# Performance work log

Measured on AMD Instinct MI355X. Metric: run time of the kernel, lower is better.

The kernel has to match this reference:

```python
import jax, jax.numpy as jnp
import numpy as np

N_NODES = 50000
N_EDGES = 1600000
IN_DIM = 1024
MID_DIM = 256


def setup_inputs() -> dict:
    key = jax.random.key(0)
    k1, k2, k3, k4 = jax.random.split(key, 4)
    x = jax.random.normal(k1, (N_NODES, IN_DIM), dtype=jnp.float32)
    edge_index = jax.random.randint(k2, (2, N_EDGES), 0, N_NODES, dtype=jnp.int64)
    # Glorot-style init like PyG GCNConv
    W1 = jax.random.normal(k3, (IN_DIM, MID_DIM), dtype=jnp.float32) * (2.0 / (IN_DIM + MID_DIM)) ** 0.5
    W2 = jax.random.normal(k4, (MID_DIM, IN_DIM), dtype=jnp.float32) * (2.0 / (MID_DIM + IN_DIM)) ** 0.5
    b1 = jnp.zeros((MID_DIM,), dtype=jnp.float32)
    b2 = jnp.zeros((IN_DIM,), dtype=jnp.float32)
    return {"x": x, "edge_index": edge_index, "W1": W1, "b1": b1, "W2": W2, "b2": b2}


def _gcn_conv(x, W, b, src, dst, norm, n):
    # PyG GCNConv: linear transform first, then normalized neighbor sum, then bias.
    xw = x @ W                                   # [N, F_out]
    msg = xw[src] * norm[:, None]                # gather + scale, [E+N, F_out]
    out = jax.ops.segment_sum(msg, dst, num_segments=n)
    return out + b


def reference(x, edge_index, W1, b1, W2, b2):
    n = x.shape[0]
    loops = jnp.arange(n, dtype=edge_index.dtype)
    src = jnp.concatenate([edge_index[0], loops])
    dst = jnp.concatenate([edge_index[1], loops])
    # symmetric normalization with self-loops: D^-1/2 (A+I) D^-1/2
    deg = jax.ops.segment_sum(jnp.ones_like(dst, dtype=x.dtype), dst, num_segments=n)
    dis = jnp.where(deg > 0, jax.lax.rsqrt(jnp.maximum(deg, 1.0)), 0.0)
    norm = dis[src] * dis[dst]                   # [E+N]
    h = jax.nn.relu(_gcn_conv(x, W1, b1, src, dst, norm, n))
    # F.dropout(training=False) is identity at inference
    out = _gcn_conv(h, W2, b2, src, dst, norm, n)
    return out
```

## Files before the change

kernel.cpp:

```cpp
#include <hip/hip_runtime.h>

typedef unsigned short u16;
typedef u16 u16x8 __attribute__((ext_vector_type(8)));
typedef u16 u16x4 __attribute__((ext_vector_type(4)));
typedef short s16x8 __attribute__((ext_vector_type(8)));
typedef float f32x4 __attribute__((ext_vector_type(4)));

__device__ __forceinline__ float b2f(u16 u) {
  unsigned int v = ((unsigned int)u) << 16;
  return __builtin_bit_cast(float, v);
}
__device__ __forceinline__ u16 f2b(float f) {
  unsigned int u = __builtin_bit_cast(unsigned int, f);
  u += 0x7FFFu + ((u >> 16) & 1u);
  return (u16)(u >> 16);
}

__device__ __forceinline__ void gld16(void* lds, const void* g) {
  __builtin_amdgcn_global_load_lds(
      (const __attribute__((address_space(1))) void*)g,
      (__attribute__((address_space(3))) void*)lds, 16, 0, 0);
}

__global__ void deg_kernel(const int* __restrict__ dst, int* __restrict__ deg, int E, int n) {
  int e = blockIdx.x * 256 + threadIdx.x;
  if (e < E) {
    int d = dst[e];
    d = min(max(d, 0), n - 1);
    atomicAdd(&deg[d], 1);
  }
}

__global__ void dis_kernel(const int* __restrict__ deg, float* __restrict__ dis, int n) {
  int i = blockIdx.x * 256 + threadIdx.x;
  if (i < n) dis[i] = 1.0f / sqrtf((float)(deg[i] + 1));
}

__global__ __launch_bounds__(256) void scanA(const int* __restrict__ cnt, int* __restrict__ bsum, int n) {
  __shared__ int s[256];
  int t = threadIdx.x, i = blockIdx.x * 256 + t;
  s[t] = (i < n) ? cnt[i] : 0;
  __syncthreads();
  for (int off = 128; off > 0; off >>= 1) {
    if (t < off) s[t] += s[t + off];
    __syncthreads();
  }
  if (t == 0) bsum[blockIdx.x] = s[0];
}

__global__ __launch_bounds__(256) void scanB(int* __restrict__ bsum, int nb) {
  __shared__ int s[256];
  int t = threadIdx.x;
  int v = (t < nb) ? bsum[t] : 0;
  s[t] = v;
  __syncthreads();
  for (int off = 1; off < 256; off <<= 1) {
    int x = (t >= off) ? s[t - off] : 0;
    __syncthreads();
    s[t] += x;
    __syncthreads();
  }
  if (t < nb) bsum[t] = s[t] - v;
}

__global__ __launch_bounds__(256) void scanC(const int* __restrict__ cnt, const int* __restrict__ bsum,
                                             int* __restrict__ rowp, int n) {
  __shared__ int s[256];
  int t = threadIdx.x, i = blockIdx.x * 256 + t;
  int v = (i < n) ? cnt[i] : 0;
  s[t] = v;
  __syncthreads();
  for (int off = 1; off < 256; off <<= 1) {
    int x = (t >= off) ? s[t - off] : 0;
    __syncthreads();
    s[t] += x;
    __syncthreads();
  }
  if (i < n) rowp[i + 1] = bsum[blockIdx.x] + s[t];
  if (i == 0) rowp[0] = 0;
}

__global__ void fill_kernel(const int* __restrict__ src, const int* __restrict__ dst,
                            const int* __restrict__ rowp, int* __restrict__ fill,
                            const float* __restrict__ dis, int* __restrict__ csr_s,
                            float* __restrict__ csr_w, int E, int n) {
  int e = blockIdx.x * 256 + threadIdx.x;
  if (e < E) {
    int s = src[e]; s = min(max(s, 0), n - 1);
    int d = dst[e]; d = min(max(d, 0), n - 1);
    int pos = rowp[d] + atomicAdd(&fill[d], 1);
    csr_s[pos] = s;
    csr_w[pos] = dis[s] * dis[d];
  }
}

__global__ void transpose_cvt(const float* __restrict__ in, u16* __restrict__ out, int K, int N) {
  int idx = blockIdx.x * 256 + threadIdx.x;
  if (idx < K * N) {
    int k = idx / N, nn = idx - k * N;
    out[(size_t)nn * K + k] = f2b(in[idx]);
  }
}

template <bool A_F32, bool OUT_F32>
__global__ __launch_bounds__(256) void gemm_m97(const void* __restrict__ Ap,
                                                const u16* __restrict__ BT,
                                                const float* __restrict__ bias,
                                                void* __restrict__ Cp, int M, int N, int K) {
  constexpr int ABYTES = A_F32 ? 16384 : 8192;
  __shared__ alignas(16) unsigned char smem[ABYTES + 8192];
  unsigned char* Asm = smem;
  unsigned char* Bsm = smem + ABYTES;

  const int tid = threadIdx.x;
  const int m0 = blockIdx.y * 128, n0 = blockIdx.x * 128;
  const int lane = tid & 63, wv = tid >> 6;
  const int wr = (wv >> 1) * 64, wc = (wv & 1) * 64;
  const int q = lane >> 4, l = lane & 15;
  f32x4 acc[4][4] = {};

  constexpr int NA = A_F32 ? 4 : 2;
  constexpr size_t AB = A_F32 ? 4 : 2;
  const char* a_src[NA];
  const char* b_src[2];
#pragma unroll
  for (int i = 0; i < NA; i++) {
    int c = tid + i * 256;
    int r, lb;
    if (A_F32) {
      r = c >> 3;
      int sb = (c & 7) * 16;
      lb = sb ^ ((r & 7) << 4);
    } else {
      r = c >> 2;
      int sb = (c & 3) * 16;
      lb = sb ^ ((r & 3) << 4);
    }
    int gr = m0 + r;
    if (gr > M - 1) gr = M - 1;
    a_src[i] = (const char*)Ap + (size_t)gr * K * AB + lb;
  }
#pragma unroll
  for (int i = 0; i < 2; i++) {
    int c = tid + i * 256;
    int r = c >> 2;
    int sb = (c & 3) * 16;
    int lb = sb ^ ((r & 3) << 4);
    b_src[i] = (const char*)BT + (size_t)(n0 + r) * K * 2 + lb;
  }

  for (int kt = 0; kt < K; kt += 32) {
#pragma unroll
    for (int i = 0; i < NA; i++)
      gld16(Asm + (tid + i * 256) * 16, a_src[i] + (size_t)kt * AB);
#pragma unroll
    for (int i = 0; i < 2; i++)
      gld16(Bsm + (tid + i * 256) * 16, b_src[i] + (size_t)kt * 2);
    __syncthreads();

    s16x8 af[4], bf[4];
    if (A_F32) {
#pragma unroll
      for (int mi = 0; mi < 4; mi++) {
        int R = wr + mi * 16 + l;
        int xr = (R & 7) << 4;
        const char* rb = (const char*)Asm + R * 128;
        float4 lo = *(const float4*)(rb + ((q * 32) ^ xr));
        float4 hi = *(const float4*)(rb + ((q * 32 + 16) ^ xr));
        unsigned int d0, d1, d2, d3;
        asm("v_cvt_pk_bf16_f32 %0, %1, %2" : "=v"(d0) : "v"(lo.x), "v"(lo.y));
        asm("v_cvt_pk_bf16_f32 %0, %1, %2" : "=v"(d1) : "v"(lo.z), "v"(lo.w));
        asm("v_cvt_pk_bf16_f32 %0, %1, %2" : "=v"(d2) : "v"(hi.x), "v"(hi.y));
        asm("v_cvt_pk_bf16_f32 %0, %1, %2" : "=v"(d3) : "v"(hi.z), "v"(hi.w));
        int4 di;
        di.x = (int)d0; di.y = (int)d1; di.z = (int)d2; di.w = (int)d3;
        af[mi] = __builtin_bit_cast(s16x8, di);
      }
    } else {
#pragma unroll
      for (int mi = 0; mi < 4; mi++) {
        int R = wr + mi * 16 + l;
        af[mi] = *(const s16x8*)((const char*)Asm + R * 64 + ((q * 16) ^ ((R & 3) << 4)));
      }
    }
#pragma unroll
    for (int ni = 0; ni < 4; ni++) {
      int C = wc + ni * 16 + l;
      bf[ni] = *(const s16x8*)((const char*)Bsm + C * 64 + ((q * 16) ^ ((C & 3) << 4)));
    }

#pragma unroll
    for (int mi = 0; mi < 4; mi++)
#pragma unroll
      for (int ni = 0; ni < 4; ni++)
        acc[mi][ni] = __builtin_amdgcn_mfma_f32_16x16x32_bf16(af[mi], bf[ni], acc[mi][ni], 0, 0, 0);
    __syncthreads();
  }

#pragma unroll
  for (int ni = 0; ni < 4; ni++) {
    int col = n0 + wc + ni * 16 + l;
    float bv = bias ? bias[col] : 0.f;
#pragma unroll
    for (int mi = 0; mi < 4; mi++) {
#pragma unroll
      for (int j = 0; j < 4; j++) {
        int row = m0 + wr + mi * 16 + q * 4 + j;
        if (row < M) {
          float v = acc[mi][ni][j] + bv;
          if (OUT_F32)
            ((float*)Cp)[(size_t)row * N + col] = v;
          else
            ((u16*)Cp)[(size_t)row * N + col] = f2b(v);
        }
      }
    }
  }
}

template <bool RELU>
__global__ __launch_bounds__(256) void agg_kernel(const u16* __restrict__ tab,
                                                  const int* __restrict__ rowp,
                                                  const int* __restrict__ csr_s,
                                                  const float* __restrict__ csr_w,
                                                  const float* __restrict__ dis,
                                                  const float* __restrict__ bias,
                                                  u16* __restrict__ out, int n) {
  int wv = threadIdx.x >> 6, lane = threadIdx.x & 63;
  int node = blockIdx.x * 4 + wv;
  if (node >= n) return;
  int f0 = lane * 4;
  float sw = dis[node];
  sw *= sw;
  u16x4 v = *(const u16x4*)&tab[(size_t)node * 256 + f0];
  float a0 = sw * b2f(v[0]), a1 = sw * b2f(v[1]), a2 = sw * b2f(v[2]), a3 = sw * b2f(v[3]);
  int e0 = rowp[node], e1 = rowp[node + 1];
  int e = e0;
  for (; e + 4 <= e1; e += 4) {
    int s0 = csr_s[e], s1 = csr_s[e + 1], s2 = csr_s[e + 2], s3 = csr_s[e + 3];
    float w0 = csr_w[e], w1 = csr_w[e + 1], w2 = csr_w[e + 2], w3 = csr_w[e + 3];
    u16x4 u0 = *(const u16x4*)&tab[(size_t)s0 * 256 + f0];
    u16x4 u1 = *(const u16x4*)&tab[(size_t)s1 * 256 + f0];
    u16x4 u2 = *(const u16x4*)&tab[(size_t)s2 * 256 + f0];
    u16x4 u3 = *(const u16x4*)&tab[(size_t)s3 * 256 + f0];
    a0 += w0 * b2f(u0[0]) + w1 * b2f(u1[0]) + w2 * b2f(u2[0]) + w3 * b2f(u3[0]);
    a1 += w0 * b2f(u0[1]) + w1 * b2f(u1[1]) + w2 * b2f(u2[1]) + w3 * b2f(u3[1]);
    a2 += w0 * b2f(u0[2]) + w1 * b2f(u1[2]) + w2 * b2f(u2[2]) + w3 * b2f(u3[2]);
    a3 += w0 * b2f(u0[3]) + w1 * b2f(u1[3]) + w2 * b2f(u2[3]) + w3 * b2f(u3[3]);
  }
  for (; e < e1; e++) {
    int s = csr_s[e];
    float w = csr_w[e];
    u16x4 u = *(const u16x4*)&tab[(size_t)s * 256 + f0];
    a0 += w * b2f(u[0]);
    a1 += w * b2f(u[1]);
    a2 += w * b2f(u[2]);
    a3 += w * b2f(u[3]);
  }
  if (RELU) {
    a0 = fmaxf(a0 + bias[f0 + 0], 0.f);
    a1 = fmaxf(a1 + bias[f0 + 1], 0.f);
    a2 = fmaxf(a2 + bias[f0 + 2], 0.f);
    a3 = fmaxf(a3 + bias[f0 + 3], 0.f);
  }
  u16x4 o;
  o[0] = f2b(a0); o[1] = f2b(a1); o[2] = f2b(a2); o[3] = f2b(a3);
  *(u16x4*)&out[(size_t)node * 256 + f0] = o;
}

extern "C" void kernel_launch(void* const* d_in, const int* in_sizes, int n_in,
                              void* d_out, int out_size, void* d_ws, size_t ws_size,
                              hipStream_t stream) {
  const float* x  = (const float*)d_in[0];
  const int*   ei = (const int*)d_in[1];
  const float* W1 = (const float*)d_in[2];
  const float* b1 = (const float*)d_in[3];
  const float* W2 = (const float*)d_in[4];
  const float* b2 = (const float*)d_in[5];

  const int MID = in_sizes[3];
  const int IN  = in_sizes[5];
  const int n   = in_sizes[0] / IN;
  const int E   = in_sizes[1] / 2;
  const int* srcv = ei;
  const int* dstv = ei + E;

  char* w = (char*)d_ws;
  size_t off = 0;
  auto alloc = [&](size_t bytes) -> void* {
    void* p = w + off;
    off += (bytes + 255) & ~(size_t)255;
    return p;
  };
  int*   deg   = (int*)alloc((size_t)n * 4);
  int*   rowp  = (int*)alloc((size_t)(n + 1) * 4);
  int*   fill  = (int*)alloc((size_t)n * 4);
  int*   bsum  = (int*)alloc(1024);
  int*   csr_s = (int*)alloc((size_t)E * 4);
  float* csr_w = (float*)alloc((size_t)E * 4);
  float* dis   = (float*)alloc((size_t)n * 4);
  u16*   W1T   = (u16*)alloc((size_t)IN * MID * 2);
  u16*   W2T   = (u16*)alloc((size_t)IN * MID * 2);
  u16*   xw    = (u16*)alloc((size_t)n * MID * 2);
  u16*   h     = (u16*)alloc((size_t)n * MID * 2);
  u16*   ah    = xw;

  hipMemsetAsync(deg, 0, (size_t)n * 4, stream);
  hipMemsetAsync(fill, 0, (size_t)n * 4, stream);

  transpose_cvt<<<(IN * MID + 255) / 256, 256, 0, stream>>>(W1, W1T, IN, MID);
  transpose_cvt<<<(IN * MID + 255) / 256, 256, 0, stream>>>(W2, W2T, MID, IN);

  const int nb = (n + 255) / 256;
  deg_kernel<<<(E + 255) / 256, 256, 0, stream>>>(dstv, deg, E, n);
  dis_kernel<<<nb, 256, 0, stream>>>(deg, dis, n);
  scanA<<<nb, 256, 0, stream>>>(deg, bsum, n);
  scanB<<<1, 256, 0, stream>>>(bsum, nb);
  scanC<<<nb, 256, 0, stream>>>(deg, bsum, rowp, n);
  fill_kernel<<<(E + 255) / 256, 256, 0, stream>>>(srcv, dstv, rowp, fill, dis, csr_s, csr_w, E, n);

  dim3 g1(MID / 128, (n + 127) / 128);
  gemm_m97<true, false><<<g1, 256, 0, stream>>>(x, W1T, nullptr, xw, n, MID, IN);
  agg_kernel<true><<<(n + 3) / 4, 256, 0, stream>>>(xw, rowp, csr_s, csr_w, dis, b1, h, n);
  agg_kernel<false><<<(n + 3) / 4, 256, 0, stream>>>(h, rowp, csr_s, csr_w, dis, nullptr, ah, n);
  dim3 g2(IN / 128, (n + 127) / 128);
  gemm_m97<false, true><<<g2, 256, 0, stream>>>(ah, W2T, b2, d_out, n, IN, MID);
}
```

Baseline: 891.2 us.

## Replace 4-wave 128x128 GEMM with single-wave 64x64 tiles without block barriers

Both dense GEMMs move from 256-thread blocks computing 128x128 tiles to one-wave blocks computing 64x64 tiles. Because a block is now a single wave, the __syncthreads barriers are replaced by an explicit vmcnt wait plus a scheduling barrier. The aim is to cut barrier stalls and raise the number of independently scheduled blocks. In exchange, each tile reuses loaded data less, so the large fp32 input and the weights are fetched more times. There is also still no double buffering, so loads and MFMA work stay serialized within each wave.

```diff
diff --git a/kernel.cpp b/kernel.cpp
--- a/kernel.cpp
+++ b/kernel.cpp
@@ -103,29 +103,27 @@
 }
 
 template <bool A_F32, bool OUT_F32>
-__global__ __launch_bounds__(256) void gemm_m97(const void* __restrict__ Ap,
-                                                const u16* __restrict__ BT,
-                                                const float* __restrict__ bias,
-                                                void* __restrict__ Cp, int M, int N, int K) {
-  constexpr int ABYTES = A_F32 ? 16384 : 8192;
-  __shared__ alignas(16) unsigned char smem[ABYTES + 8192];
+__global__ __launch_bounds__(64) void gemm_w64(const void* __restrict__ Ap,
+                                               const u16* __restrict__ BT,
+                                               const float* __restrict__ bias,
+                                               void* __restrict__ Cp, int M, int N, int K) {
+  constexpr int ABYTES = A_F32 ? 8192 : 4096;
+  __shared__ alignas(16) unsigned char smem[ABYTES + 4096];
   unsigned char* Asm = smem;
   unsigned char* Bsm = smem + ABYTES;
 
-  const int tid = threadIdx.x;
-  const int m0 = blockIdx.y * 128, n0 = blockIdx.x * 128;
-  const int lane = tid & 63, wv = tid >> 6;
-  const int wr = (wv >> 1) * 64, wc = (wv & 1) * 64;
+  const int lane = threadIdx.x;
+  const int m0 = blockIdx.y * 64, n0 = blockIdx.x * 64;
   const int q = lane >> 4, l = lane & 15;
   f32x4 acc[4][4] = {};
 
-  constexpr int NA = A_F32 ? 4 : 2;
+  constexpr int NA = A_F32 ? 8 : 4;
   constexpr size_t AB = A_F32 ? 4 : 2;
   const char* a_src[NA];
-  const char* b_src[2];
+  const char* b_src[4];
 #pragma unroll
   for (int i = 0; i < NA; i++) {
-    int c = tid + i * 256;
+    int c = lane + i * 64;
     int r, lb;
     if (A_F32) {
       r = c >> 3;
@@ -141,8 +139,8 @@
     a_src[i] = (const char*)Ap + (size_t)gr * K * AB + lb;
   }
 #pragma unroll
-  for (int i = 0; i < 2; i++) {
-    int c = tid + i * 256;
+  for (int i = 0; i < 4; i++) {
+    int c = lane + i * 64;
     int r = c >> 2;
     int sb = (c & 3) * 16;
     int lb = sb ^ ((r & 3) << 4);
@@ -152,17 +150,18 @@
   for (int kt = 0; kt < K; kt += 32) {
 #pragma unroll
     for (int i = 0; i < NA; i++)
-      gld16(Asm + (tid + i * 256) * 16, a_src[i] + (size_t)kt * AB);
-#pragma unroll
-    for (int i = 0; i < 2; i++)
-      gld16(Bsm + (tid + i * 256) * 16, b_src[i] + (size_t)kt * 2);
-    __syncthreads();
+      gld16(Asm + (lane + i * 64) * 16, a_src[i] + (size_t)kt * AB);
+#pragma unroll
+    for (int i = 0; i < 4; i++)
+      gld16(Bsm + (lane + i * 64) * 16, b_src[i] + (size_t)kt * 2);
+    asm volatile("s_waitcnt vmcnt(0)" ::: "memory");
+    __builtin_amdgcn_sched_barrier(0);
 
     s16x8 af[4], bf[4];
     if (A_F32) {
 #pragma unroll
       for (int mi = 0; mi < 4; mi++) {
-        int R = wr + mi * 16 + l;
+        int R = mi * 16 + l;
         int xr = (R & 7) << 4;
         const char* rb = (const char*)Asm + R * 128;
         float4 lo = *(const float4*)(rb + ((q * 32) ^ xr));
@@ -179,13 +178,13 @@
     } else {
 #pragma unroll
       for (int mi = 0; mi < 4; mi++) {
-        int R = wr + mi * 16 + l;
+        int R = mi * 16 + l;
         af[mi] = *(const s16x8*)((const char*)Asm + R * 64 + ((q * 16) ^ ((R & 3) << 4)));
       }
     }
 #pragma unroll
     for (int ni = 0; ni < 4; ni++) {
-      int C = wc + ni * 16 + l;
+      int C = ni * 16 + l;
       bf[ni] = *(const s16x8*)((const char*)Bsm + C * 64 + ((q * 16) ^ ((C & 3) << 4)));
     }
 
@@ -194,18 +193,17 @@
 #pragma unroll
       for (int ni = 0; ni < 4; ni++)
         acc[mi][ni] = __builtin_amdgcn_mfma_f32_16x16x32_bf16(af[mi], bf[ni], acc[mi][ni], 0, 0, 0);
-    __syncthreads();
   }
 
 #pragma unroll
   for (int ni = 0; ni < 4; ni++) {
-    int col = n0 + wc + ni * 16 + l;
+    int col = n0 + ni * 16 + l;
     float bv = bias ? bias[col] : 0.f;
 #pragma unroll
     for (int mi = 0; mi < 4; mi++) {
 #pragma unroll
       for (int j = 0; j < 4; j++) {
-        int row = m0 + wr + mi * 16 + q * 4 + j;
+        int row = m0 + mi * 16 + q * 4 + j;
         if (row < M) {
           float v = acc[mi][ni][j] + bv;
           if (OUT_F32)
@@ -319,10 +317,10 @@
   scanC<<<nb, 256, 0, stream>>>(deg, bsum, rowp, n);
   fill_kernel<<<(E + 255) / 256, 256, 0, stream>>>(srcv, dstv, rowp, fill, dis, csr_s, csr_w, E, n);
 
-  dim3 g1(MID / 128, (n + 127) / 128);
-  gemm_m97<true, false><<<g1, 256, 0, stream>>>(x, W1T, nullptr, xw, n, MID, IN);
+  dim3 g1(MID / 64, (n + 63) / 64);
+  gemm_w64<true, false><<<g1, 64, 0, stream>>>(x, W1T, nullptr, xw, n, MID, IN);
   agg_kernel<true><<<(n + 3) / 4, 256, 0, stream>>>(xw, rowp, csr_s, csr_w, dis, b1, h, n);
   agg_kernel<false><<<(n + 3) / 4, 256, 0, stream>>>(h, rowp, csr_s, csr_w, dis, nullptr, ah, n);
-  dim3 g2(IN / 128, (n + 127) / 128);
-  gemm_m97<false, true><<<g2, 256, 0, stream>>>(ah, W2T, b2, d_out, n, IN, MID);
-}
+  dim3 g2(IN / 64, (n + 63) / 64);
+  gemm_w64<false, true><<<g2, 64, 0, stream>>>(ah, W2T, b2, d_out, n, IN, MID);
+}
```

Result: slower. 923.2 us (+3.6%).
